# Optimization experiments

Hardware: AMD Instinct MI355X
Metric: run time of the kernel (lower is better)

Reference implementation:

```python
import jax, jax.numpy as jnp
import numpy as np

N = 50000      # nodes
E = 500000     # edges (avg degree 10)
G = 64         # graphs (events)
IN = 7
H = 64
EPS = 1e-5


def setup_inputs() -> dict:
    key = jax.random.key(0)
    ks = iter(jax.random.split(key, 64))
    d = {}
    d["x"] = jax.random.normal(next(ks), (N, IN), jnp.float32)
    d["edge_index"] = jax.random.randint(next(ks), (2, E), 0, N, dtype=jnp.int32)
    d["batch"] = jnp.sort(jax.random.randint(next(ks), (N,), 0, G, dtype=jnp.int32))
    dims = [(IN, H), (H, 2 * H), (2 * H, 4 * H)]
    for i, (ic, oc) in enumerate(dims, 1):
        d[f"b{i}_W1"] = jax.random.normal(next(ks), (2 * ic, oc), jnp.float32) * 0.05
        d[f"b{i}_b1"] = jnp.zeros((oc,), jnp.float32)
        d[f"b{i}_g1"] = jnp.ones((oc,), jnp.float32)
        d[f"b{i}_beta1"] = jnp.zeros((oc,), jnp.float32)
        d[f"b{i}_W2"] = jax.random.normal(next(ks), (oc, oc), jnp.float32) * 0.05
        d[f"b{i}_b2"] = jnp.zeros((oc,), jnp.float32)
        d[f"b{i}_g2"] = jnp.ones((oc,), jnp.float32)
        d[f"b{i}_beta2"] = jnp.zeros((oc,), jnp.float32)
    d["head_W1"] = jax.random.normal(next(ks), (4 * H, 2 * H), jnp.float32) * 0.05
    d["head_b1"] = jnp.zeros((2 * H,), jnp.float32)
    d["head_W2"] = jax.random.normal(next(ks), (2 * H, 2), jnp.float32) * 0.05
    d["head_b2"] = jnp.zeros((2,), jnp.float32)
    return d


def _bn(h, g, b):
    # BatchNorm1d in training mode: batch statistics over edge dim
    m = h.mean(axis=0)
    v = h.var(axis=0)
    return (h - m) * jax.lax.rsqrt(v + EPS) * g + b


def _edgeconv(x, src, dst, W1, b1, g1, be1, W2, b2, g2, be2):
    # PyG EdgeConv: message = MLP(cat[x_i, x_j - x_i]), aggregated at target i=dst
    xi = x[dst]                                   # [E, C]
    xj = x[src]                                   # [E, C]
    e = jnp.concatenate([xi, xj - xi], axis=-1)   # [E, 2C]
    h = jax.nn.relu(_bn(e @ W1 + b1, g1, be1))
    h = jax.nn.relu(_bn(h @ W2 + b2, g2, be2))
    s = jax.ops.segment_sum(h, dst, num_segments=N)
    cnt = jax.ops.segment_sum(jnp.ones((h.shape[0],), h.dtype), dst, num_segments=N)
    return s / jnp.maximum(cnt, 1.0)[:, None]     # mean aggregation


def reference(x, edge_index, batch,
              b1_W1, b1_b1, b1_g1, b1_beta1, b1_W2, b1_b2, b1_g2, b1_beta2,
              b2_W1, b2_b1, b2_g1, b2_beta1, b2_W2, b2_b2, b2_g2, b2_beta2,
              b3_W1, b3_b1, b3_g1, b3_beta1, b3_W2, b3_b2, b3_g2, b3_beta2,
              head_W1, head_b1, head_W2, head_b2):
    src, dst = edge_index[0], edge_index[1]
    h = _edgeconv(x, src, dst, b1_W1, b1_b1, b1_g1, b1_beta1, b1_W2, b1_b2, b1_g2, b1_beta2)
    h = _edgeconv(h, src, dst, b2_W1, b2_b1, b2_g1, b2_beta1, b2_W2, b2_b2, b2_g2, b2_beta2)
    h = _edgeconv(h, src, dst, b3_W1, b3_b1, b3_g1, b3_beta1, b3_W2, b3_b2, b3_g2, b3_beta2)
    # global mean pool per graph
    s = jax.ops.segment_sum(h, batch, num_segments=G)
    cnt = jax.ops.segment_sum(jnp.ones((N,), h.dtype), batch, num_segments=G)
    g = s / jnp.maximum(cnt, 1.0)[:, None]        # [G, 256]
    # head (dropout is identity in eval)
    z = jax.nn.relu(g @ head_W1 + head_b1)
    return z @ head_W2 + head_b2                  # [G, 2]
```

## Files before the change

### kernel.cpp

```cpp
#include <hip/hip_runtime.h>
#include <stdint.h>

constexpr int NN = 50000;
constexpr int NE = 500000;
constexpr int NG = 64;
constexpr float BN_EPS = 1e-5f;

typedef __attribute__((ext_vector_type(8))) short bf16x8;
typedef __attribute__((ext_vector_type(4))) float f32x4;

__device__ inline float bf2f(unsigned short u) {
    return __uint_as_float(((unsigned int)u) << 16);
}
__device__ inline unsigned short f2bf_rne(float f) {
    unsigned int u = __float_as_uint(f);
    unsigned int r = (u + 0x7fffu + ((u >> 16) & 1u)) >> 16;
    return (unsigned short)r;
}

template<int CPT> __device__ inline void load_row(const float* p, float* o) {
    if constexpr (CPT == 2) { float2 v = *(const float2*)p; o[0]=v.x; o[1]=v.y; }
    else if constexpr (CPT == 4) { float4 v = *(const float4*)p; o[0]=v.x; o[1]=v.y; o[2]=v.z; o[3]=v.w; }
    else { load_row<4>(p, o); load_row<4>(p+4, o+4); }
}
template<int CPT> __device__ inline void store_row(float* p, const float* v) {
    if constexpr (CPT == 2) { *(float2*)p = make_float2(v[0], v[1]); }
    else if constexpr (CPT == 4) { *(float4*)p = make_float4(v[0], v[1], v[2], v[3]); }
    else { store_row<4>(p, v); store_row<4>(p+4, v+4); }
}

__global__ void k_zero16(uint4* p, int n) {
    int i = blockIdx.x * 256 + threadIdx.x;
    if (i < n) p[i] = uint4{0u, 0u, 0u, 0u};
}

__global__ void k_diag(float* out, int n, float val) {
    int i = blockIdx.x * 256 + threadIdx.x;
    if (i < n) out[i] = val;
}

__global__ void k_deg(const int* __restrict__ dst, int* __restrict__ degi) {
    int e = blockIdx.x * 256 + threadIdx.x;
    if (e < NE) atomicAdd(&degi[dst[e]], 1);
}

__global__ void k_scan(const int* __restrict__ degi, int* __restrict__ rowptr) {
    __shared__ int buf[1024];
    __shared__ int carry_s;
    const int tid = threadIdx.x;
    if (tid == 0) carry_s = 0;
    __syncthreads();
    for (int base = 0; base < NN; base += 1024) {
        int i = base + tid;
        int v = (i < NN) ? degi[i] : 0;
        buf[tid] = v;
        __syncthreads();
        for (int off = 1; off < 1024; off <<= 1) {
            int t = (tid >= off) ? buf[tid - off] : 0;
            __syncthreads();
            buf[tid] += t;
            __syncthreads();
        }
        if (i < NN) rowptr[i] = carry_s + buf[tid] - v;
        __syncthreads();
        if (tid == 0) carry_s += buf[1023];
        __syncthreads();
    }
    if (tid == 0) rowptr[NN] = carry_s;
}

__global__ void k_fill(const int* __restrict__ dst, const int* __restrict__ rowptr,
                       int* __restrict__ cursor, int* __restrict__ eidx) {
    int e = blockIdx.x * 256 + threadIdx.x;
    if (e < NE) {
        int d = dst[e];
        int p = atomicAdd(&cursor[d], 1);
        eidx[rowptr[d] + p] = e;
    }
}

__global__ void k_grange(const int* __restrict__ batch, int* __restrict__ gse) {
    int n = blockIdx.x * 256 + threadIdx.x;
    if (n >= NN) return;
    int b = batch[n];
    if (n == 0 || batch[n-1] != b) gse[b] = n;
    if (n == NN-1 || batch[n+1] != b) gse[NG + b] = n + 1;
}

template<int OC>
__global__ void k_bnfin(const float* __restrict__ st, const float* __restrict__ g,
                        const float* __restrict__ be, float* __restrict__ dv) {
    int c = threadIdx.x;
    const float invE = 1.0f / (float)NE;
    float m = st[c] * invE;
    float v = st[OC + c] * invE - m * m;
    float sc = g[c] * rsqrtf(v + BN_EPS);
    dv[c] = sc;
    dv[OC + c] = be[c] - m * sc;
}

template<int OC>
__global__ void k_packW(const float* __restrict__ W,
                        unsigned short* __restrict__ Wph, unsigned short* __restrict__ Wpl) {
    constexpr int NT = OC / 16;
    const int l = threadIdx.x;
    const int ktnt = blockIdx.x;
    const int n = (ktnt % NT) * 16 + (l & 15);
    const int kbase = (ktnt / NT) * 32 + (l >> 4) * 8;
    size_t fo = ((size_t)ktnt * 64 + l) * 8;
    #pragma unroll
    for (int b = 0; b < 8; b++) {
        float w = W[(size_t)(kbase + b) * OC + n];
        unsigned short h = f2bf_rne(w);
        Wph[fo + b] = h;
        Wpl[fo + b] = f2bf_rne(w - bf2f(h));
    }
}

template<int CIN, int OC>
__global__ __launch_bounds__(256) void k_nodeproj(
    const float* __restrict__ x, const float* __restrict__ W1,
    const float* __restrict__ b1, float* __restrict__ A, float* __restrict__ Bn)
{
    constexpr int SP = CIN + 1;
    constexpr int CPT = OC / 32;
    __shared__ float xs[32 * SP];
    const int t = threadIdx.x;
    const int n0 = blockIdx.x * 32;
    {
        const int el = t >> 3, l8 = t & 7;
        int n = n0 + el; if (n >= NN) n = NN - 1;
        const float* xp = x + (size_t)n * CIN;
        for (int k = l8; k < CIN; k += 8) xs[el * SP + k] = xp[k];
    }
    __syncthreads();
    const int tx = t & 31, ty = t >> 5;
    float accA[4][CPT], accB[4][CPT];
    #pragma unroll
    for (int i = 0; i < 4; i++)
        #pragma unroll
        for (int j = 0; j < CPT; j++) { accA[i][j] = 0.f; accB[i][j] = 0.f; }

    const float* Wa = W1 + tx * CPT;
    const float* Wb = W1 + (size_t)CIN * OC + tx * CPT;
    for (int k = 0; k < CIN; k++) {
        float wa[CPT], wb[CPT];
        load_row<CPT>(Wa + (size_t)k * OC, wa);
        load_row<CPT>(Wb + (size_t)k * OC, wb);
        #pragma unroll
        for (int i = 0; i < 4; i++) {
            float ev = xs[(ty * 4 + i) * SP + k];
            #pragma unroll
            for (int j = 0; j < CPT; j++) {
                accA[i][j] = fmaf(ev, wa[j] - wb[j], accA[i][j]);
                accB[i][j] = fmaf(ev, wb[j], accB[i][j]);
            }
        }
    }
    float bs[CPT];
    load_row<CPT>(b1 + tx * CPT, bs);
    #pragma unroll
    for (int i = 0; i < 4; i++) {
        const int n = n0 + ty * 4 + i;
        if (n < NN) {
            float va[CPT];
            #pragma unroll
            for (int j = 0; j < CPT; j++) va[j] = accA[i][j] + bs[j];
            store_row<CPT>(A  + (size_t)n * OC + tx * CPT, va);
            store_row<CPT>(Bn + (size_t)n * OC + tx * CPT, accB[i]);
        }
    }
}

template<int OC>
__global__ __launch_bounds__(256) void k_stats1(
    const float* __restrict__ A, const float* __restrict__ Bn,
    const int* __restrict__ src, const int* __restrict__ dst,
    const int* __restrict__ eidx, float* __restrict__ stats)
{
    constexpr int CPT = OC / 32;
    __shared__ float reds[4 * OC];
    __shared__ float redq[4 * OC];
    const int t = threadIdx.x;
    const int l32 = t & 31, grp = t >> 5;
    float s[CPT], q[CPT];
    #pragma unroll
    for (int j = 0; j < CPT; j++) { s[j] = 0.f; q[j] = 0.f; }
    for (int i = blockIdx.x * 8 + grp; i < NE; i += 8192) {
        const int e = eidx[i];
        float av[CPT], bv[CPT];
        load_row<CPT>(A  + (size_t)dst[e] * OC + l32 * CPT, av);
        load_row<CPT>(Bn + (size_t)src[e] * OC + l32 * CPT, bv);
        #pragma unroll
        for (int j = 0; j < CPT; j++) {
            float h = av[j] + bv[j];
            s[j] += h; q[j] += h * h;
        }
    }
    #pragma unroll
    for (int j = 0; j < CPT; j++) {
        s[j] += __shfl_down(s[j], 32);
        q[j] += __shfl_down(q[j], 32);
    }
    const int w = t >> 6, lane = t & 63;
    if (lane < 32) {
        #pragma unroll
        for (int j = 0; j < CPT; j++) {
            reds[w * OC + lane * CPT + j] = s[j];
            redq[w * OC + lane * CPT + j] = q[j];
        }
    }
    __syncthreads();
    for (int c = t; c < OC; c += 256) {
        float S = reds[c] + reds[OC + c] + reds[2 * OC + c] + reds[3 * OC + c];
        float Q = redq[c] + redq[OC + c] + redq[2 * OC + c] + redq[3 * OC + c];
        atomicAdd(&stats[c], S);
        atomicAdd(&stats[OC + c], Q);
    }
}

template<int OC, int MODE>
__global__ __launch_bounds__(256, 2) void k_efuse(
    const float* __restrict__ A, const float* __restrict__ Bn,
    const int* __restrict__ src, const int* __restrict__ dst,
    const int* __restrict__ eidx,
    const unsigned short* __restrict__ Wph, const unsigned short* __restrict__ Wpl,
    const float* __restrict__ b2,
    const float* __restrict__ dv1, float* __restrict__ stats,
    const float* __restrict__ dv2, float* __restrict__ xout)
{
    constexpr int ETL = 128;
    constexpr int NT = OC / 16;
    constexpr int NTW = NT / 2;
    constexpr int NCH = OC / 64;
    constexpr int SROWS = 8192 / OC;
    constexpr int NSTRIP = ETL / SROWS;
    constexpr int YSTR = OC + 4;
    constexpr int YB = SROWS * YSTR * 4;
    constexpr int TB = (MODE == 0) ? 16384 : 32768;
    constexpr int SMB = (MODE == 1 && YB > TB) ? YB : TB;

    __shared__ __align__(16) unsigned char smem[SMB];
    __shared__ int sdst_s[ETL], ssrc_s[ETL];

    const int t = threadIdx.x;
    const int e0 = blockIdx.x * ETL;
    const int valid = (NE - e0 < ETL) ? (NE - e0) : ETL;

    if (t < ETL) {
        int dn = -1, sn = -1;
        if (t < valid) { int e = eidx[e0 + t]; dn = dst[e]; sn = src[e]; }
        sdst_s[t] = dn; ssrc_s[t] = sn;
    }
    __syncthreads();

    const int lane = t & 63, wave = t >> 6;
    const int rg = wave >> 1, ch = wave & 1;
    const int lr = lane & 15, lg = lane >> 4;

    f32x4 acc[4][NTW];
    #pragma unroll
    for (int m = 0; m < 4; m++)
        #pragma unroll
        for (int n = 0; n < NTW; n++) acc[m][n] = (f32x4){0.f, 0.f, 0.f, 0.f};

    const int brow = t >> 1, bhf = t & 1;
    const bool rvalid = (brow < valid);
    const float* Arow = rvalid ? (A  + (size_t)sdst_s[brow] * OC + bhf * 32) : nullptr;
    const float* Brow = rvalid ? (Bn + (size_t)ssrc_s[brow] * OC + bhf * 32) : nullptr;

    float4 pa[8], pb[8];
    if (rvalid) {
        #pragma unroll
        for (int i = 0; i < 8; i++) {
            pa[i] = *(const float4*)(Arow + i * 4);
            pb[i] = *(const float4*)(Brow + i * 4);
        }
    }

    for (int kc = 0; kc < NCH; kc++) {
        {
            const int gc0 = kc * 64 + bhf * 32;
            if (rvalid) {
                #pragma unroll
                for (int i = 0; i < 8; i++) {
                    float4 a  = pa[i];
                    float4 b  = pb[i];
                    float4 sc = *(const float4*)(dv1 + gc0 + i * 4);
                    float4 sh = *(const float4*)(dv1 + OC + gc0 + i * 4);
                    float tv[4];
                    tv[0] = fmaxf(fmaf(a.x + b.x, sc.x, sh.x), 0.f);
                    tv[1] = fmaxf(fmaf(a.y + b.y, sc.y, sh.y), 0.f);
                    tv[2] = fmaxf(fmaf(a.z + b.z, sc.z, sh.z), 0.f);
                    tv[3] = fmaxf(fmaf(a.w + b.w, sc.w, sh.w), 0.f);
                    unsigned short hv[4];
                    #pragma unroll
                    for (int j = 0; j < 4; j++) hv[j] = f2bf_rne(tv[j]);
                    const int byt = (brow * 128 + bhf * 64 + i * 8) ^ ((brow & 7) << 4);
                    *(ushort4*)(smem + byt) = *(ushort4*)hv;
                    if constexpr (MODE == 1) {
                        unsigned short lv[4];
                        #pragma unroll
                        for (int j = 0; j < 4; j++) lv[j] = f2bf_rne(tv[j] - bf2f(hv[j]));
                        *(ushort4*)(smem + 16384 + byt) = *(ushort4*)lv;
                    }
                }
            } else {
                const ushort4 z = ushort4{0, 0, 0, 0};
                #pragma unroll
                for (int i = 0; i < 8; i++) {
                    const int byt = (brow * 128 + bhf * 64 + i * 8) ^ ((brow & 7) << 4);
                    *(ushort4*)(smem + byt) = z;
                    if constexpr (MODE == 1) *(ushort4*)(smem + 16384 + byt) = z;
                }
            }
        }
        __syncthreads();

        if (kc + 1 < NCH && rvalid) {
            const int goff = (kc + 1) * 64;
            #pragma unroll
            for (int i = 0; i < 8; i++) {
                pa[i] = *(const float4*)(Arow + goff + i * 4);
                pb[i] = *(const float4*)(Brow + goff + i * 4);
            }
        }

        #pragma unroll
        for (int kt2 = 0; kt2 < 2; kt2++) {
            bf16x8 ah[4], al[4];
            #pragma unroll
            for (int m = 0; m < 4; m++) {
                const int r = rg * 64 + m * 16 + lr;
                const int byt = (r * 128 + kt2 * 64 + lg * 16) ^ ((r & 7) << 4);
                ah[m] = *(const bf16x8*)(smem + byt);
                if constexpr (MODE == 1) al[m] = *(const bf16x8*)(smem + 16384 + byt);
            }
            #pragma unroll
            for (int n = 0; n < NTW; n++) {
                const size_t fo = ((size_t)((kc * 2 + kt2) * NT + ch * NTW + n) * 64 + lane) * 8;
                bf16x8 wh = *(const bf16x8*)(Wph + fo);
                if constexpr (MODE == 0) {
                    #pragma unroll
                    for (int m = 0; m < 4; m++)
                        acc[m][n] = __builtin_amdgcn_mfma_f32_16x16x32_bf16(ah[m], wh, acc[m][n], 0, 0, 0);
                } else {
                    bf16x8 wl = *(const bf16x8*)(Wpl + fo);
                    #pragma unroll
                    for (int m = 0; m < 4; m++) {
                        acc[m][n] = __builtin_amdgcn_mfma_f32_16x16x32_bf16(ah[m], wh, acc[m][n], 0, 0, 0);
                        acc[m][n] = __builtin_amdgcn_mfma_f32_16x16x32_bf16(ah[m], wl, acc[m][n], 0, 0, 0);
                        acc[m][n] = __builtin_amdgcn_mfma_f32_16x16x32_bf16(al[m], wh, acc[m][n], 0, 0, 0);
                    }
                }
            }
        }
        __syncthreads();
    }

    if constexpr (MODE == 0) {
        #pragma unroll
        for (int n = 0; n < NTW; n++) {
            const int col = ch * (OC / 2) + n * 16 + lr;
            const float bb = b2[col];
            float s = 0.f, q = 0.f;
            #pragma unroll
            for (int m = 0; m < 4; m++) {
                const int rbase = rg * 64 + m * 16 + lg * 4;
                #pragma unroll
                for (int e = 0; e < 4; e++) {
                    float h = (rbase + e < valid) ? (acc[m][n][e] + bb) : 0.f;
                    s += h; q += h * h;
                }
            }
            s += __shfl_xor(s, 16); s += __shfl_xor(s, 32);
            q += __shfl_xor(q, 16); q += __shfl_xor(q, 32);
            if (lg == 0) {
                atomicAdd(&stats[col], s);
                atomicAdd(&stats[OC + col], q);
            }
        }
    } else {
        float* yt = (float*)smem;
        const int acol = t % OC;
        const int aseg = t / OC;
        #pragma unroll
        for (int s = 0; s < NSTRIP; s++) {
            const int r0 = s * SROWS;
            #pragma unroll
            for (int m = 0; m < 4; m++) {
                const int base = rg * 64 + m * 16;
                if (base >= r0 && base < r0 + SROWS) {
                    #pragma unroll
                    for (int n = 0; n < NTW; n++) {
                        const int col = ch * (OC / 2) + n * 16 + lr;
                        const float bb = b2[col], scv = dv2[col], shv = dv2[OC + col];
                        #pragma unroll
                        for (int e = 0; e < 4; e++) {
                            const int rl = base - r0 + lg * 4 + e;
                            yt[rl * YSTR + col] = fmaxf(fmaf(acc[m][n][e] + bb, scv, shv), 0.f);
                        }
                    }
                }
            }
            __syncthreads();
            {
                const int rbeg = aseg * 32;
                float a = 0.f; int cur = -1;
                for (int r = 0; r < 32; r++) {
                    const int gr = r0 + rbeg + r;
                    if (gr >= valid) break;
                    const int nd = sdst_s[gr];
                    if (nd != cur) {
                        if (cur >= 0) atomicAdd(&xout[(size_t)cur * OC + acol], a);
                        cur = nd; a = 0.f;
                    }
                    a += yt[(rbeg + r) * YSTR + acol];
                }
                if (cur >= 0) atomicAdd(&xout[(size_t)cur * OC + acol], a);
            }
            __syncthreads();
        }
    }
}

template<int OC>
__global__ __launch_bounds__(256) void k_div(float* __restrict__ xout,
                                             const int* __restrict__ degi) {
    constexpr int CPT = OC / 32;
    const int tx = threadIdx.x & 31;
    const int n = blockIdx.x * 8 + (threadIdx.x >> 5);
    if (n >= NN) return;
    const float inv = 1.0f / fmaxf((float)degi[n], 1.0f);
    float v[CPT];
    load_row<CPT>(xout + (size_t)n * OC + tx * CPT, v);
    #pragma unroll
    for (int j = 0; j < CPT; j++) v[j] *= inv;
    store_row<CPT>(xout + (size_t)n * OC + tx * CPT, v);
}

__global__ void k_pool(const float* __restrict__ x3, const int* __restrict__ gse,
                       float* __restrict__ pooled) {
    const int g = blockIdx.x, c = threadIdx.x;
    const int beg = gse[g], end = gse[NG + g];
    float s = 0.f;
    for (int n = beg; n < end; n++) s += x3[(size_t)n * 256 + c];
    pooled[g * 256 + c] = s / fmaxf((float)(end - beg), 1.0f);
}

__global__ void k_head(const float* __restrict__ pooled,
                       const float* __restrict__ W1, const float* __restrict__ b1,
                       const float* __restrict__ W2, const float* __restrict__ b2,
                       float* __restrict__ out) {
    __shared__ float gv[256];
    __shared__ float z[128];
    const int g = blockIdx.x;
    gv[threadIdx.x] = pooled[g * 256 + threadIdx.x];
    __syncthreads();
    if (threadIdx.x < 128) {
        const int c = threadIdx.x;
        float s = b1[c];
        for (int k = 0; k < 256; k++) s = fmaf(gv[k], W1[k * 128 + c], s);
        z[c] = fmaxf(s, 0.f);
    }
    __syncthreads();
    if (threadIdx.x < 2) {
        const int o = threadIdx.x;
        float s = b2[o];
        for (int k = 0; k < 128; k++) s = fmaf(z[k], W2[k * 2 + o], s);
        out[g * 2 + o] = s;
    }
}

template<int CIN, int OC>
static void run_block(const float* xin, const float* const* Q,
                      float* A, float* B, const int* src, const int* dst,
                      const int* eidx, const unsigned short* Wph, const unsigned short* Wpl,
                      float* st, float* dv, const int* degi,
                      float* xout, hipStream_t s)
{
    const int EG = (NE + 127) / 128;
    k_nodeproj<CIN, OC><<<(NN + 31) / 32, 256, 0, s>>>(xin, Q[0], Q[1], A, B);
    k_stats1<OC><<<1024, 256, 0, s>>>(A, B, src, dst, eidx, st);
    k_bnfin<OC><<<1, OC, 0, s>>>(st, Q[2], Q[3], dv);
    k_efuse<OC, 0><<<EG, 256, 0, s>>>(A, B, src, dst, eidx, Wph, Wpl, Q[5], dv, st + 512, nullptr, nullptr);
    k_bnfin<OC><<<1, OC, 0, s>>>(st + 512, Q[6], Q[7], dv + 512);
    k_zero16<<<((NN * OC / 4) + 255) / 256, 256, 0, s>>>((uint4*)xout, NN * OC / 4);
    k_efuse<OC, 1><<<EG, 256, 0, s>>>(A, B, src, dst, eidx, Wph, Wpl, Q[5], dv, nullptr, dv + 512, xout);
    k_div<OC><<<(NN + 7) / 8, 256, 0, s>>>(xout, degi);
}

extern "C" void kernel_launch(void* const* d_in, const int* in_sizes, int n_in,
                              void* d_out, int out_size, void* d_ws, size_t ws_size,
                              hipStream_t stream)
{
    (void)in_sizes; (void)n_in;
    const float* x = (const float*)d_in[0];
    const int* ei = (const int*)d_in[1];
    const int* src = ei;
    const int* dst = ei + NE;
    const int* batch = (const int*)d_in[2];
    const float* P[28];
    for (int i = 0; i < 28; i++) P[i] = (const float*)d_in[3 + i];
    float* out = (float*)d_out;

    size_t offs[18];
    {
        size_t o = 0;
        auto take = [&](size_t bytes) -> size_t {
            size_t r = o; o = (o + bytes + 255) & ~(size_t)255; return r;
        };
        offs[0] = take((size_t)NN * 256 * 4);
        offs[1] = take((size_t)NN * 256 * 4);
        offs[2] = take((size_t)NN * 256 * 4);
        offs[3] = take((size_t)NN * 128 * 4);
        offs[4] = o;
        offs[5] = take((size_t)NN * 4);
        offs[6] = take((size_t)NN * 4);
        offs[7] = take(3 * 1024 * 4);
        offs[8] = take(2 * NG * 4);
        offs[9] = o;
        offs[10] = take((size_t)(NN + 1) * 4);
        offs[11] = take((size_t)NE * 4);
        offs[12] = take(3 * 1024 * 4);
        offs[13] = take((size_t)NG * 256 * 4);
        offs[14] = take((64*64 + 128*128 + 256*256) * 2);
        offs[15] = take((64*64 + 128*128 + 256*256) * 2);
        offs[16] = o;
        if (ws_size < o) {
            float val = 1000.0f + (float)(ws_size >> 20);
            k_diag<<<(out_size + 255) / 256, 256, 0, stream>>>(out, out_size, val);
            return;
        }
    }

    char* W = (char*)d_ws;
    float* A  = (float*)(W + offs[0]);
    float* B  = (float*)(W + offs[1]);
    float* xa = (float*)(W + offs[2]);
    float* xb = (float*)(W + offs[3]);
    int* degi = (int*)(W + offs[5]);
    int* cursor = (int*)(W + offs[6]);
    float* stats = (float*)(W + offs[7]);
    int* gse = (int*)(W + offs[8]);
    int* rowptr = (int*)(W + offs[10]);
    int* eidx = (int*)(W + offs[11]);
    float* dv = (float*)(W + offs[12]);
    float* pooled = (float*)(W + offs[13]);
    unsigned short* Wph = (unsigned short*)(W + offs[14]);
    unsigned short* Wpl = (unsigned short*)(W + offs[15]);
    unsigned short* Wph1 = Wph,            * Wpl1 = Wpl;
    unsigned short* Wph2 = Wph + 64*64,    * Wpl2 = Wpl + 64*64;
    unsigned short* Wph3 = Wph2 + 128*128, * Wpl3 = Wpl2 + 128*128;

    int nz = (int)((offs[9] - offs[4]) / 16);
    k_zero16<<<(nz + 255) / 256, 256, 0, stream>>>((uint4*)(W + offs[4]), nz);

    k_deg<<<(NE + 255) / 256, 256, 0, stream>>>(dst, degi);
    k_scan<<<1, 1024, 0, stream>>>(degi, rowptr);
    k_fill<<<(NE + 255) / 256, 256, 0, stream>>>(dst, rowptr, cursor, eidx);
    k_grange<<<(NN + 255) / 256, 256, 0, stream>>>(batch, gse);

    k_packW<64> <<<(64/32)*(64/16),   64, 0, stream>>>(P[4],  Wph1, Wpl1);
    k_packW<128><<<(128/32)*(128/16), 64, 0, stream>>>(P[12], Wph2, Wpl2);
    k_packW<256><<<(256/32)*(256/16), 64, 0, stream>>>(P[20], Wph3, Wpl3);

    run_block<7,   64>(x,  P + 0,  A, B, src, dst, eidx, Wph1, Wpl1, stats + 0,    dv + 0,    degi, xa, stream);
    run_block<64, 128>(xa, P + 8,  A, B, src, dst, eidx, Wph2, Wpl2, stats + 1024, dv + 1024, degi, xb, stream);
    run_block<128,256>(xb, P + 16, A, B, src, dst, eidx, Wph3, Wpl3, stats + 2048, dv + 2048, degi, xa, stream);

    k_pool<<<NG, 256, 0, stream>>>(xa, gse, pooled);
    k_head<<<NG, 256, 0, stream>>>(pooled, P[24], P[25], P[26], P[27], out);
}
```

Measured before the change: 2.862 ms.

## Split edge-fused MLP tiles across eight waves and drop register prefetch

```diff
diff --git a/kernel.cpp b/kernel.cpp
--- a/kernel.cpp
+++ b/kernel.cpp
@@ -220,7 +220,7 @@
 }
 
 template<int OC, int MODE>
-__global__ __launch_bounds__(256, 2) void k_efuse(
+__global__ __launch_bounds__(512, 3) void k_efuse(
     const float* __restrict__ A, const float* __restrict__ Bn,
     const int* __restrict__ src, const int* __restrict__ dst,
     const int* __restrict__ eidx,
@@ -231,7 +231,7 @@
 {
     constexpr int ETL = 128;
     constexpr int NT = OC / 16;
-    constexpr int NTW = NT / 2;
+    constexpr int NTW = NT / 4;
     constexpr int NCH = OC / 64;
     constexpr int SROWS = 8192 / OC;
     constexpr int NSTRIP = ETL / SROWS;
@@ -239,6 +239,8 @@
     constexpr int YB = SROWS * YSTR * 4;
     constexpr int TB = (MODE == 0) ? 16384 : 32768;
     constexpr int SMB = (MODE == 1 && YB > TB) ? YB : TB;
+    constexpr int NSEG = 512 / OC;
+    constexpr int RSEG = SROWS / NSEG;
 
     __shared__ __align__(16) unsigned char smem[SMB];
     __shared__ int sdst_s[ETL], ssrc_s[ETL];
@@ -255,7 +257,7 @@
     __syncthreads();
 
     const int lane = t & 63, wave = t >> 6;
-    const int rg = wave >> 1, ch = wave & 1;
+    const int rg = wave >> 2, ch = wave & 3;
     const int lr = lane & 15, lg = lane >> 4;
 
     f32x4 acc[4][NTW];
@@ -264,28 +266,19 @@
         #pragma unroll
         for (int n = 0; n < NTW; n++) acc[m][n] = (f32x4){0.f, 0.f, 0.f, 0.f};
 
-    const int brow = t >> 1, bhf = t & 1;
+    const int brow = t >> 2, q = t & 3;
     const bool rvalid = (brow < valid);
-    const float* Arow = rvalid ? (A  + (size_t)sdst_s[brow] * OC + bhf * 32) : nullptr;
-    const float* Brow = rvalid ? (Bn + (size_t)ssrc_s[brow] * OC + bhf * 32) : nullptr;
-
-    float4 pa[8], pb[8];
-    if (rvalid) {
-        #pragma unroll
-        for (int i = 0; i < 8; i++) {
-            pa[i] = *(const float4*)(Arow + i * 4);
-            pb[i] = *(const float4*)(Brow + i * 4);
-        }
-    }
+    const float* Arow = rvalid ? (A  + (size_t)sdst_s[brow] * OC + q * 16) : nullptr;
+    const float* Brow = rvalid ? (Bn + (size_t)ssrc_s[brow] * OC + q * 16) : nullptr;
 
     for (int kc = 0; kc < NCH; kc++) {
         {
-            const int gc0 = kc * 64 + bhf * 32;
+            const int gc0 = kc * 64 + q * 16;
             if (rvalid) {
                 #pragma unroll
-                for (int i = 0; i < 8; i++) {
-                    float4 a  = pa[i];
-                    float4 b  = pb[i];
+                for (int i = 0; i < 4; i++) {
+                    float4 a  = *(const float4*)(Arow + kc * 64 + i * 4);
+                    float4 b  = *(const float4*)(Brow + kc * 64 + i * 4);
                     float4 sc = *(const float4*)(dv1 + gc0 + i * 4);
                     float4 sh = *(const float4*)(dv1 + OC + gc0 + i * 4);
                     float tv[4];
@@ -296,7 +289,7 @@
                     unsigned short hv[4];
                     #pragma unroll
                     for (int j = 0; j < 4; j++) hv[j] = f2bf_rne(tv[j]);
-                    const int byt = (brow * 128 + bhf * 64 + i * 8) ^ ((brow & 7) << 4);
+                    const int byt = (brow * 128 + q * 32 + i * 8) ^ ((brow & 7) << 4);
                     *(ushort4*)(smem + byt) = *(ushort4*)hv;
                     if constexpr (MODE == 1) {
                         unsigned short lv[4];
@@ -308,23 +301,14 @@
             } else {
                 const ushort4 z = ushort4{0, 0, 0, 0};
                 #pragma unroll
-                for (int i = 0; i < 8; i++) {
-                    const int byt = (brow * 128 + bhf * 64 + i * 8) ^ ((brow & 7) << 4);
+                for (int i = 0; i < 4; i++) {
+                    const int byt = (brow * 128 + q * 32 + i * 8) ^ ((brow & 7) << 4);
                     *(ushort4*)(smem + byt) = z;
                     if constexpr (MODE == 1) *(ushort4*)(smem + 16384 + byt) = z;
                 }
             }
         }
         __syncthreads();
-
-        if (kc + 1 < NCH && rvalid) {
-            const int goff = (kc + 1) * 64;
-            #pragma unroll
-            for (int i = 0; i < 8; i++) {
-                pa[i] = *(const float4*)(Arow + goff + i * 4);
-                pb[i] = *(const float4*)(Brow + goff + i * 4);
-            }
-        }
 
         #pragma unroll
         for (int kt2 = 0; kt2 < 2; kt2++) {
@@ -361,23 +345,23 @@
     if constexpr (MODE == 0) {
         #pragma unroll
         for (int n = 0; n < NTW; n++) {
-            const int col = ch * (OC / 2) + n * 16 + lr;
+            const int col = (ch * NTW + n) * 16 + lr;
             const float bb = b2[col];
-            float s = 0.f, q = 0.f;
+            float s = 0.f, qq = 0.f;
             #pragma unroll
             for (int m = 0; m < 4; m++) {
                 const int rbase = rg * 64 + m * 16 + lg * 4;
                 #pragma unroll
                 for (int e = 0; e < 4; e++) {
                     float h = (rbase + e < valid) ? (acc[m][n][e] + bb) : 0.f;
-                    s += h; q += h * h;
+                    s += h; qq += h * h;
                 }
             }
             s += __shfl_xor(s, 16); s += __shfl_xor(s, 32);
-            q += __shfl_xor(q, 16); q += __shfl_xor(q, 32);
+            qq += __shfl_xor(qq, 16); qq += __shfl_xor(qq, 32);
             if (lg == 0) {
                 atomicAdd(&stats[col], s);
-                atomicAdd(&stats[OC + col], q);
+                atomicAdd(&stats[OC + col], qq);
             }
         }
     } else {
@@ -393,7 +377,7 @@
                 if (base >= r0 && base < r0 + SROWS) {
                     #pragma unroll
                     for (int n = 0; n < NTW; n++) {
-                        const int col = ch * (OC / 2) + n * 16 + lr;
+                        const int col = (ch * NTW + n) * 16 + lr;
                         const float bb = b2[col], scv = dv2[col], shv = dv2[OC + col];
                         #pragma unroll
                         for (int e = 0; e < 4; e++) {
@@ -405,9 +389,9 @@
             }
             __syncthreads();
             {
-                const int rbeg = aseg * 32;
+                const int rbeg = aseg * RSEG;
                 float a = 0.f; int cur = -1;
-                for (int r = 0; r < 32; r++) {
+                for (int r = 0; r < RSEG; r++) {
                     const int gr = r0 + rbeg + r;
                     if (gr >= valid) break;
                     const int nd = sdst_s[gr];
@@ -483,10 +467,10 @@
     k_nodeproj<CIN, OC><<<(NN + 31) / 32, 256, 0, s>>>(xin, Q[0], Q[1], A, B);
     k_stats1<OC><<<1024, 256, 0, s>>>(A, B, src, dst, eidx, st);
     k_bnfin<OC><<<1, OC, 0, s>>>(st, Q[2], Q[3], dv);
-    k_efuse<OC, 0><<<EG, 256, 0, s>>>(A, B, src, dst, eidx, Wph, Wpl, Q[5], dv, st + 512, nullptr, nullptr);
+    k_efuse<OC, 0><<<EG, 512, 0, s>>>(A, B, src, dst, eidx, Wph, Wpl, Q[5], dv, st + 512, nullptr, nullptr);
     k_bnfin<OC><<<1, OC, 0, s>>>(st + 512, Q[6], Q[7], dv + 512);
     k_zero16<<<((NN * OC / 4) + 255) / 256, 256, 0, s>>>((uint4*)xout, NN * OC / 4);
-    k_efuse<OC, 1><<<EG, 256, 0, s>>>(A, B, src, dst, eidx, Wph, Wpl, Q[5], dv, nullptr, dv + 512, xout);
+    k_efuse<OC, 1><<<EG, 512, 0, s>>>(A, B, src, dst, eidx, Wph, Wpl, Q[5], dv, nullptr, dv + 512, xout);
     k_div<OC><<<(NN + 7) / 8, 256, 0, s>>>(xout, degi);
 }
 
```

Measured after the change: 2.522 ms. -11.9%, faster.
